# Kernel tuning notes

Measured on AMD Instinct MI355X. Metric: run time of the kernel, lower is better.

Reference implementation:

```python
import jax, jax.numpy as jnp
import numpy as np

B, T = 192, 50
VOCAB = 24000
EMBED = 300
HID2 = 2000          # 2*HIDDEN_SIZE
MAXOUT = 300         # DIMEN_MAXOUT_UNIT
QV = 300             # DIMEN_QUALITY_VECTOR
H2 = 100             # LSTM hidden


def setup_inputs():
    key = jax.random.key(0)
    ks = jax.random.split(key, 24)
    s = 0.02
    inp = {
        'dec_out': jax.random.normal(ks[0], (B, T, HID2), jnp.float32),
        'y': jax.random.randint(ks[1], (B, T), 0, VOCAB, jnp.int64 if jax.config.jax_enable_x64 else jnp.int32),
        'contex': jax.random.normal(ks[2], (B, T, HID2), jnp.float32),
        'embed_table': jax.random.normal(ks[3], (VOCAB, EMBED), jnp.float32) * s,
        'W1': jax.random.uniform(ks[4], (VOCAB, QV), jnp.float32),  # torch.rand
        'S_w': jax.random.normal(ks[5], (2 * MAXOUT, HID2), jnp.float32) * s,
        'S_b': jnp.zeros((2 * MAXOUT,), jnp.float32),
        'V_w': jax.random.normal(ks[6], (2 * MAXOUT, 2 * EMBED), jnp.float32) * s,
        'V_b': jnp.zeros((2 * MAXOUT,), jnp.float32),
        'C0_w': jax.random.normal(ks[7], (2 * MAXOUT, HID2), jnp.float32) * s,
        'C0_b': jnp.zeros((2 * MAXOUT,), jnp.float32),
        'W2_w': jax.random.normal(ks[8], (QV, MAXOUT), jnp.float32) * s,
        'W2_b': jnp.zeros((QV,), jnp.float32),
        'wih0': jax.random.normal(ks[9], (4 * H2, QV), jnp.float32) * s,
        'whh0': jax.random.normal(ks[10], (4 * H2, H2), jnp.float32) * s,
        'bih0': jnp.zeros((4 * H2,), jnp.float32),
        'bhh0': jnp.zeros((4 * H2,), jnp.float32),
        'wih1': jax.random.normal(ks[11], (4 * H2, H2), jnp.float32) * s,
        'whh1': jax.random.normal(ks[12], (4 * H2, H2), jnp.float32) * s,
        'bih1': jnp.zeros((4 * H2,), jnp.float32),
        'bhh1': jnp.zeros((4 * H2,), jnp.float32),
        'Wqe_w': jax.random.normal(ks[13], (1, H2), jnp.float32) * s,
        'Wqe_b': jnp.zeros((1,), jnp.float32),
    }
    return inp


def _lstm_layer(x, Wih, Whh, bih, bhh):
    # x: [B, T, D] -> outputs [B, T, H]; torch gate order i, f, g, o
    Bb = x.shape[0]
    H = Whh.shape[1]
    xT = jnp.swapaxes(x, 0, 1)  # [T, B, D]

    def step(carry, xt):
        h, c = carry
        g = xt @ Wih.T + h @ Whh.T + bih + bhh
        i, f, gg, o = jnp.split(g, 4, axis=-1)
        i = jax.nn.sigmoid(i); f = jax.nn.sigmoid(f)
        gg = jnp.tanh(gg); o = jax.nn.sigmoid(o)
        c = f * c + i * gg
        h = o * jnp.tanh(c)
        return (h, c), h

    h0 = jnp.zeros((Bb, H), x.dtype)
    (_, _), hs = jax.lax.scan(step, (h0, h0), xT)
    return jnp.swapaxes(hs, 0, 1)


def reference(dec_out, y, contex, embed_table, W1, S_w, S_b, V_w, V_b,
              C0_w, C0_b, W2_w, W2_b, wih0, whh0, bih0, bhh0,
              wih1, whh1, bih1, bhh1, Wqe_w, Wqe_b):
    Bb, Tt, _ = dec_out.shape
    embed = embed_table[y]  # [B, T, EMBED]
    idx = jnp.arange(Tt)
    li = jnp.where(idx == 0, 1, idx - 1)          # left neighbor (i==0 -> 1)
    ri = jnp.where(idx == Tt - 1, Tt - 2, idx + 1)  # right neighbor (i==T-1 -> T-2)
    tensor2 = jnp.concatenate([embed[:, li], embed[:, ri]], axis=-1)  # [B,T,600]
    t_long = (dec_out @ S_w.T + S_b) + (tensor2 @ V_w.T + V_b) + (contex @ C0_w.T + C0_b)
    # maxout over consecutive pairs: t[...,i] = max(t_long[...,2i], t_long[...,2i+1])
    t = t_long.reshape(Bb, Tt, MAXOUT, 2).max(axis=-1)
    a = t @ W2_w.T + W2_b                        # [B,T,QV]
    logits = a @ W1.T                            # [B,T,VOCAB]
    b = jax.nn.log_softmax(logits.reshape(Bb * Tt, -1), axis=1)
    quality = W1[y] * a                          # [B,T,QV]
    mask = (y == 0)
    index1 = jnp.where(mask.any(axis=1), mask.argmax(axis=1), Tt - 1)
    h = _lstm_layer(quality, wih0, whh0, bih0, bhh0)
    h = _lstm_layer(h, wih1, whh1, bih1, bhh1)   # [B,T,H2]
    s_sel = h[jnp.arange(Bb), index1]            # [B,H2]
    QE_score = jax.nn.sigmoid(s_sel @ Wqe_w.T + Wqe_b)  # [B,1]
    return (b, QE_score)
```

## Files before the change

### kernel.cpp

```cpp
#include <hip/hip_runtime.h>

typedef unsigned short u16;
typedef __attribute__((ext_vector_type(4))) float f32x4;
typedef __attribute__((ext_vector_type(8))) short bf16x8;
typedef __attribute__((ext_vector_type(4))) unsigned short u16x4;
typedef __attribute__((ext_vector_type(8))) unsigned short u16x8;

#define BT 9600
#define VOCAB 24000
#define NCB 188

__device__ __forceinline__ u16 f2b(float f){
  union { float f; unsigned u; } c; c.f = f;
  unsigned u = c.u;
  return (u16)((u + 0x7FFFu + ((u >> 16) & 1u)) >> 16);
}
__device__ __forceinline__ float b2f(u16 v){
  union { unsigned u; float f; } c; c.u = ((unsigned)v) << 16;
  return c.f;
}

#define GLD16(g, l) __builtin_amdgcn_global_load_lds( \
    (__attribute__((address_space(1))) void*)(g), \
    (__attribute__((address_space(3))) void*)(l), 16, 0, 0)

__device__ __forceinline__ void gemm_core(
    const u16* __restrict__ A, const u16* __restrict__ B,
    int K, int brow, int bcol, u16* As, u16* Bs, f32x4 acc[4][4])
{
  const int tid  = threadIdx.x & 255;
  const int w    = tid >> 6;
  const int lane = tid & 63;
  const int wm = w >> 1, wn = w & 1;

  const f32x4 fz = {0.f, 0.f, 0.f, 0.f};
  #pragma unroll
  for (int m = 0; m < 4; ++m)
    #pragma unroll
    for (int n = 0; n < 4; ++n) acc[m][n] = fz;

  const int nkt = K >> 6;

  auto stage = [&](int kt, int buf) {
    #pragma unroll
    for (int i = 0; i < 4; ++i) {
      int gl  = i * 256 + tid;
      int row = gl >> 3;
      int g   = (gl & 7) ^ (row & 7);
      const u16* ga = A + (size_t)(brow + row) * K + (kt << 6) + (g << 3);
      GLD16(ga, As + buf * 8192 + (size_t)(i * 256 + w * 64) * 8);
      const u16* gb = B + (size_t)(bcol + row) * K + (kt << 6) + (g << 3);
      GLD16(gb, Bs + buf * 8192 + (size_t)(i * 256 + w * 64) * 8);
    }
  };

  stage(0, 0);
  int cur = 0;
  for (int kt = 0; kt < nkt; ++kt) {
    if (kt + 1 < nkt) {
      stage(kt + 1, cur ^ 1);
      asm volatile("s_waitcnt vmcnt(8)" ::: "memory");
    } else {
      asm volatile("s_waitcnt vmcnt(0)" ::: "memory");
    }
    __builtin_amdgcn_s_barrier();
    asm volatile("" ::: "memory");
    const u16* Ab = As + cur * 8192;
    const u16* Bb = Bs + cur * 8192;
    #pragma unroll
    for (int kk = 0; kk < 2; ++kk) {
      bf16x8 af[4], bf[4];
      #pragma unroll
      for (int m = 0; m < 4; ++m) {
        int row = wm * 64 + m * 16 + (lane & 15);
        int g   = (kk * 4 + (lane >> 4)) ^ (row & 7);
        af[m] = *(const bf16x8*)(Ab + row * 64 + g * 8);
      }
      #pragma unroll
      for (int n = 0; n < 4; ++n) {
        int row = wn * 64 + n * 16 + (lane & 15);
        int g   = (kk * 4 + (lane >> 4)) ^ (row & 7);
        bf[n] = *(const bf16x8*)(Bb + row * 64 + g * 8);
      }
      #pragma unroll
      for (int m = 0; m < 4; ++m)
        #pragma unroll
        for (int n = 0; n < 4; ++n)
          acc[m][n] = __builtin_amdgcn_mfma_f32_16x16x32_bf16(af[m], bf[n], acc[m][n], 0, 0, 0);
    }
    asm volatile("" ::: "memory");
    __builtin_amdgcn_s_barrier();
    cur ^= 1;
  }
}

__device__ __forceinline__ void proj_epilogue(
    f32x4 acc[4][4], int brow, int bcol,
    const float* __restrict__ b1, const float* __restrict__ b2,
    float* __restrict__ out)
{
  int tid = threadIdx.x & 255;
  int lane = tid & 63, w = tid >> 6;
  int wm = w >> 1, wn = w & 1;
  #pragma unroll
  for (int m = 0; m < 4; ++m)
    #pragma unroll
    for (int n = 0; n < 4; ++n)
      #pragma unroll
      for (int r = 0; r < 4; ++r) {
        int row = brow + wm * 64 + m * 16 + ((lane >> 4) << 2) + r;
        int col = bcol + wn * 64 + n * 16 + (lane & 15);
        if (col < 400)
          out[(size_t)row * 400 + col] = acc[m][n][r] + b1[col] + b2[col];
      }
}

__device__ __forceinline__ void prep_main_body(
    const float* __restrict__ dec, const float* __restrict__ ctx,
    u16* __restrict__ Xcat, int tid)
{
  if (tid >= 9600 * 500) return;
  int r = tid / 500, k8 = (tid % 500) * 8;
  const float* src = (k8 < 2000) ? dec + (size_t)r * 2000 + k8
                                 : ctx + (size_t)r * 2000 + (k8 - 2000);
  const float4* s4 = (const float4*)src;
  float4 v0 = s4[0], v1 = s4[1];
  u16x8 o;
  o[0] = f2b(v0.x); o[1] = f2b(v0.y); o[2] = f2b(v0.z); o[3] = f2b(v0.w);
  o[4] = f2b(v1.x); o[5] = f2b(v1.y); o[6] = f2b(v1.z); o[7] = f2b(v1.w);
  *(u16x8*)(Xcat + (size_t)r * 4608 + k8) = o;
}

__device__ __forceinline__ void prep_emb_body(
    const int* __restrict__ y, const float* __restrict__ etab,
    u16* __restrict__ Xcat, int tid)
{
  if (tid >= 9600 * 152) return;
  int r = tid / 152, u = tid % 152;
  u16* xr = Xcat + (size_t)r * 4608;
  if (u >= 150) {
    int base = (u == 150) ? 4300 : 4604;
    u16x4 z; z[0] = 0; z[1] = 0; z[2] = 0; z[3] = 0;
    *(u16x4*)(xr + base) = z;
    return;
  }
  int t = r % 50;
  int side = u / 75, j4 = (u % 75) * 4;
  int tt = (side == 0) ? (t == 0 ? 1 : t - 1) : (t == 49 ? 48 : t + 1);
  int tok = y[r - t + tt];
  float4 v = *(const float4*)(etab + (size_t)tok * 300 + j4);
  u16x4 o; o[0] = f2b(v.x); o[1] = f2b(v.y); o[2] = f2b(v.z); o[3] = f2b(v.w);
  *(u16x4*)(xr + (side == 0 ? 4000 : 4304) + j4) = o;
}

__device__ __forceinline__ void wcat_body(
    const float* __restrict__ Sw, const float* __restrict__ C0w, const float* __restrict__ Vw,
    const float* __restrict__ Sb, const float* __restrict__ Vb, const float* __restrict__ C0b,
    u16* __restrict__ Wcat, float* __restrict__ biasc, int tid)
{
  if (tid >= 640 * 4608) return;
  int n = tid / 4608, k = tid % 4608;
  float v = 0.f;
  if (n < 600) {
    if (k < 2000)                  v = Sw[n * 2000 + k];
    else if (k < 4000)             v = C0w[n * 2000 + (k - 2000)];
    else if (k < 4300)             v = Vw[n * 600 + (k - 4000)];
    else if (k >= 4304 && k < 4604) v = Vw[n * 600 + 300 + (k - 4304)];
  }
  Wcat[tid] = f2b(v);
  if (k == 0) biasc[n] = (n < 600) ? (Sb[n] + Vb[n] + C0b[n]) : 0.f;
}

__device__ __forceinline__ void conv_body(
    const float* __restrict__ src, u16* __restrict__ dst,
    int srows, int scols, int drows, int dcols4, int tid)
{
  if (tid >= drows * dcols4) return;
  int r = tid / dcols4, c4 = (tid % dcols4) * 4;
  u16x4 o; o[0] = 0; o[1] = 0; o[2] = 0; o[3] = 0;
  if (r < srows && c4 < scols) {
    float4 v = *(const float4*)(src + (size_t)r * scols + c4);
    o[0] = f2b(v.x); o[1] = f2b(v.y); o[2] = f2b(v.z); o[3] = f2b(v.w);
  }
  *(u16x4*)(dst + (size_t)r * (dcols4 * 4) + c4) = o;
}

__global__ __launch_bounds__(256) void k_prep_all(
    const float* __restrict__ dec, const float* __restrict__ ctx,
    const int* __restrict__ y, const float* __restrict__ etab,
    const float* __restrict__ Sw, const float* __restrict__ C0w,
    const float* __restrict__ Vw, const float* __restrict__ Sb,
    const float* __restrict__ Vb, const float* __restrict__ C0b,
    const float* __restrict__ W1, const float* __restrict__ W2w,
    const float* __restrict__ wih0, const float* __restrict__ wih1,
    u16* __restrict__ Xcat, u16* __restrict__ Wcat, float* __restrict__ biasc,
    u16* __restrict__ W1b, u16* __restrict__ W2b,
    u16* __restrict__ wih0b, u16* __restrict__ wih1b)
{
  int bid = blockIdx.x, th = threadIdx.x;
  if (bid < 18750)      prep_main_body(dec, ctx, Xcat, bid * 256 + th);
  else if (bid < 24450) prep_emb_body(y, etab, Xcat, (bid - 18750) * 256 + th);
  else if (bid < 35970) wcat_body(Sw, C0w, Vw, Sb, Vb, C0b, Wcat, biasc, (bid - 24450) * 256 + th);
  else if (bid < 43490) conv_body(W1,   W1b,   24000, 300, 24064, 80, (bid - 35970) * 256 + th);
  else if (bid < 43610) conv_body(W2w,  W2b,   300,   300, 384,   80, (bid - 43490) * 256 + th);
  else if (bid < 43770) conv_body(wih0, wih0b, 400,   300, 512,   80, (bid - 43610) * 256 + th);
  else                  conv_body(wih1, wih1b, 400,   100, 512,   32, (bid - 43770) * 256 + th);
}

__global__ __launch_bounds__(256) void k_gemm_tlong(
    const u16* __restrict__ Xcat, const u16* __restrict__ Wcat,
    const float* __restrict__ biasc, u16* __restrict__ tb)
{
  __shared__ u16 As[16384], Bs[16384];
  f32x4 acc[4][4];
  int L = blockIdx.x;
  int xcd = L & 7, s = L >> 3;
  int yy = (s / 5) * 8 + xcd;
  int xx = s % 5;
  if (yy >= 75) return;
  int brow = yy * 128, bcol = xx * 128;
  gemm_core(Xcat, Wcat, 4608, brow, bcol, As, Bs, acc);
  int lane = threadIdx.x & 63, w = threadIdx.x >> 6;
  int wm = w >> 1, wn = w & 1;
  #pragma unroll
  for (int m = 0; m < 4; ++m)
    #pragma unroll
    for (int n = 0; n < 4; ++n)
      #pragma unroll
      for (int r = 0; r < 4; ++r) {
        int row = brow + wm * 64 + m * 16 + ((lane >> 4) << 2) + r;
        int col = bcol + wn * 64 + n * 16 + (lane & 15);
        float v = acc[m][n][r] + biasc[col];
        float o = __shfl_xor(v, 1);
        float t = fmaxf(v, o);
        if ((lane & 1) == 0)
          tb[(size_t)row * 320 + (col >> 1)] = f2b(t);
      }
}

__global__ __launch_bounds__(256) void k_gemm_a(
    const u16* __restrict__ tb, const u16* __restrict__ W2b,
    const float* __restrict__ W2bias, const float* __restrict__ W1,
    const int* __restrict__ y, u16* __restrict__ ab, u16* __restrict__ qb)
{
  __shared__ u16 As[16384], Bs[16384];
  f32x4 acc[4][4];
  int brow = blockIdx.y * 128, bcol = blockIdx.x * 128;
  gemm_core(tb, W2b, 320, brow, bcol, As, Bs, acc);
  int lane = threadIdx.x & 63, w = threadIdx.x >> 6;
  int wm = w >> 1, wn = w & 1;
  #pragma unroll
  for (int m = 0; m < 4; ++m)
    #pragma unroll
    for (int n = 0; n < 4; ++n)
      #pragma unroll
      for (int r = 0; r < 4; ++r) {
        int row = brow + wm * 64 + m * 16 + ((lane >> 4) << 2) + r;
        int col = bcol + wn * 64 + n * 16 + (lane & 15);
        if (col < 320) {
          float bias = (col < 300) ? W2bias[col] : 0.f;
          float a = acc[m][n][r] + bias;
          ab[(size_t)row * 320 + col] = f2b(a);
          float q = 0.f;
          if (col < 300) {
            int yv = y[row];
            q = a * W1[(size_t)yv * 300 + col];
          }
          qb[(size_t)row * 320 + col] = f2b(q);
        }
      }
}

__global__ __launch_bounds__(256) void k_s1(
    const u16* __restrict__ ab, const u16* __restrict__ W1b,
    u16* __restrict__ lb, float* __restrict__ part,
    const u16* __restrict__ qb, const u16* __restrict__ wih0b,
    const float* __restrict__ bih0, const float* __restrict__ bhh0,
    float* __restrict__ xp0)
{
  __shared__ u16 smem[32768];
  __shared__ float rowsum[128][2];
  f32x4 acc[4][4];
  int bid = blockIdx.x;
  if (bid < 300) {
    int brow = (bid / 4) * 128, bcol = (bid % 4) * 128;
    gemm_core(qb, wih0b, 320, brow, bcol, smem, smem + 16384, acc);
    proj_epilogue(acc, brow, bcol, bih0, bhh0, xp0);
    return;
  }
  int g = bid - 300;
  int brow = (g / NCB) * 128, bcol = (g % NCB) * 128;
  gemm_core(ab, W1b, 320, brow, bcol, smem, smem + 16384, acc);
  int lane = threadIdx.x & 63, w = threadIdx.x >> 6;
  int wm = w >> 1, wn = w & 1;
  #pragma unroll
  for (int m = 0; m < 4; ++m)
    #pragma unroll
    for (int r = 0; r < 4; ++r) {
      int lrow = wm * 64 + m * 16 + ((lane >> 4) << 2) + r;
      float es = 0.f;
      #pragma unroll
      for (int n = 0; n < 4; ++n) {
        int lcol = wn * 64 + n * 16 + (lane & 15);
        float v = acc[m][n][r];
        smem[lrow * 136 + lcol] = f2b(v);
        if (bcol + lcol < VOCAB) es += __expf(v);
      }
      es += __shfl_xor(es, 1); es += __shfl_xor(es, 2);
      es += __shfl_xor(es, 4); es += __shfl_xor(es, 8);
      if ((lane & 15) == 0) rowsum[lrow][wn] = es;
    }
  __syncthreads();
  if (threadIdx.x < 128)
    part[(size_t)(brow + threadIdx.x) * NCB + (g % NCB)] =
        rowsum[threadIdx.x][0] + rowsum[threadIdx.x][1];
  #pragma unroll
  for (int j = 0; j < 8; ++j) {
    int ch   = j * 256 + threadIdx.x;
    int rowl = ch >> 4;
    int c16  = (ch & 15) << 3;
    u16x8 v = *(const u16x8*)(smem + rowl * 136 + c16);
    *(u16x8*)(lb + (size_t)(brow + rowl) * 24064 + bcol + c16) = v;
  }
}

__device__ __forceinline__ void lstm0_body(
    const float* __restrict__ xp0, const float* __restrict__ whh0,
    u16* __restrict__ h0b, int b)
{
  int g = threadIdx.x;
  __shared__ float h[100];
  __shared__ float act[400];
  float wrow[100];
  if (g < 400) {
    const float4* wr = (const float4*)(whh0 + (size_t)g * 100);
    #pragma unroll
    for (int q = 0; q < 25; ++q) {
      float4 t = wr[q];
      wrow[4 * q] = t.x; wrow[4 * q + 1] = t.y; wrow[4 * q + 2] = t.z; wrow[4 * q + 3] = t.w;
    }
  }
  if (g < 100) h[g] = 0.f;
  float c = 0.f;
  __syncthreads();
  for (int t = 0; t < 50; ++t) {
    if (g < 400) {
      float s = xp0[(size_t)(b * 50 + t) * 400 + g];
      const float4* hv = (const float4*)h;
      #pragma unroll
      for (int q = 0; q < 25; ++q) {
        float4 hh = hv[q];
        s += wrow[4 * q] * hh.x + wrow[4 * q + 1] * hh.y
           + wrow[4 * q + 2] * hh.z + wrow[4 * q + 3] * hh.w;
      }
      act[g] = (g >= 200 && g < 300) ? tanhf(s) : 1.f / (1.f + __expf(-s));
    }
    __syncthreads();
    if (g < 100) {
      c = act[100 + g] * c + act[g] * act[200 + g];
      float hn = act[300 + g] * tanhf(c);
      h[g] = hn;
      h0b[(size_t)(b * 50 + t) * 128 + g] = f2b(hn);
    } else if (g < 128) {
      h0b[(size_t)(b * 50 + t) * 128 + g] = 0;
    }
    __syncthreads();
  }
}

__device__ __forceinline__ void lstm1_body(
    const float* __restrict__ xp1, const float* __restrict__ whh1,
    const int* __restrict__ y, const float* __restrict__ wqe,
    const float* __restrict__ wqeb, float* __restrict__ qout, int b)
{
  int g = threadIdx.x;
  __shared__ float h[100];
  __shared__ float act[400];
  __shared__ float hsel[100];
  __shared__ int idx1;
  float wrow[100];
  if (g < 400) {
    const float4* wr = (const float4*)(whh1 + (size_t)g * 100);
    #pragma unroll
    for (int q = 0; q < 25; ++q) {
      float4 t = wr[q];
      wrow[4 * q] = t.x; wrow[4 * q + 1] = t.y; wrow[4 * q + 2] = t.z; wrow[4 * q + 3] = t.w;
    }
  }
  if (g == 0) {
    int ix = 49;
    for (int t = 0; t < 50; ++t) { if (y[b * 50 + t] == 0) { ix = t; break; } }
    idx1 = ix;
  }
  if (g < 100) { h[g] = 0.f; hsel[g] = 0.f; }
  float c = 0.f;
  __syncthreads();
  for (int t = 0; t < 50; ++t) {
    if (g < 400) {
      float s = xp1[(size_t)(b * 50 + t) * 400 + g];
      const float4* hv = (const float4*)h;
      #pragma unroll
      for (int q = 0; q < 25; ++q) {
        float4 hh = hv[q];
        s += wrow[4 * q] * hh.x + wrow[4 * q + 1] * hh.y
           + wrow[4 * q + 2] * hh.z + wrow[4 * q + 3] * hh.w;
      }
      act[g] = (g >= 200 && g < 300) ? tanhf(s) : 1.f / (1.f + __expf(-s));
    }
    __syncthreads();
    if (g < 100) {
      c = act[100 + g] * c + act[g] * act[200 + g];
      float hn = act[300 + g] * tanhf(c);
      h[g] = hn;
      if (t == idx1) hsel[g] = hn;
    }
    __syncthreads();
  }
  if (g == 0) {
    float s = wqeb[0];
    for (int j = 0; j < 100; ++j) s += hsel[j] * wqe[j];
    qout[b] = 1.f / (1.f + __expf(-s));
  }
}

__device__ __forceinline__ void fixup_body(
    const u16* __restrict__ lb, const float* __restrict__ logl,
    float* __restrict__ out, int r0, int nrows, int bid, int nb, int nthreads)
{
  size_t i = (size_t)bid * nthreads + threadIdx.x;
  size_t stride = (size_t)nb * nthreads;
  const size_t total = (size_t)nrows * (VOCAB / 8);
  for (; i < total; i += stride) {
    size_t rowl = i / (VOCAB / 8);
    int c8 = (int)(i % (VOCAB / 8)) * 8;
    size_t row = r0 + rowl;
    float l = logl[row];
    u16x8 v = *(const u16x8*)(lb + row * 24064 + c8);
    float4 o0, o1;
    o0.x = b2f(v[0]) - l; o0.y = b2f(v[1]) - l; o0.z = b2f(v[2]) - l; o0.w = b2f(v[3]) - l;
    o1.x = b2f(v[4]) - l; o1.y = b2f(v[5]) - l; o1.z = b2f(v[6]) - l; o1.w = b2f(v[7]) - l;
    float* op = out + row * VOCAB + c8;
    *(float4*)op = o0;
    *(float4*)(op + 4) = o1;
  }
}

__global__ __launch_bounds__(512) void k_s2(
    const float* __restrict__ part, float* __restrict__ logl,
    const float* __restrict__ xp0, const float* __restrict__ whh0,
    u16* __restrict__ h0b)
{
  int bid = blockIdx.x;
  if (bid < 1200) {
    int row = bid * 8 + (threadIdx.x >> 6);
    int l = threadIdx.x & 63;
    const float* p = part + (size_t)row * NCB;
    float s = p[l] + p[l + 64] + (l < 60 ? p[l + 128] : 0.f);
    s += __shfl_xor(s, 1);  s += __shfl_xor(s, 2);  s += __shfl_xor(s, 4);
    s += __shfl_xor(s, 8);  s += __shfl_xor(s, 16); s += __shfl_xor(s, 32);
    if (l == 0) logl[row] = logf(s);
    return;
  }
  lstm0_body(xp0, whh0, h0b, bid - 1200);
}

__global__ __launch_bounds__(256) void k_s3(
    const u16* __restrict__ lb, const float* __restrict__ logl,
    float* __restrict__ out,
    const u16* __restrict__ h0b, const u16* __restrict__ wih1b,
    const float* __restrict__ bih1, const float* __restrict__ bhh1,
    float* __restrict__ xp1)
{
  int bid = blockIdx.x;
  if (bid < 3072) {
    fixup_body(lb, logl, out, 0, 6400, bid, 3072, 256);
    return;
  }
  __shared__ u16 As[16384], Bs[16384];
  f32x4 acc[4][4];
  int pb = bid - 3072;
  int brow = (pb / 4) * 128, bcol = (pb % 4) * 128;
  gemm_core(h0b, wih1b, 128, brow, bcol, As, Bs, acc);
  proj_epilogue(acc, brow, bcol, bih1, bhh1, xp1);
}

__global__ __launch_bounds__(512) void k_s4(
    const u16* __restrict__ lb, const float* __restrict__ logl,
    float* __restrict__ out,
    const float* __restrict__ xp1, const float* __restrict__ whh1,
    const int* __restrict__ y, const float* __restrict__ wqe,
    const float* __restrict__ wqeb, float* __restrict__ qout)
{
  int bid = blockIdx.x;
  if (bid < 192) {
    lstm1_body(xp1, whh1, y, wqe, wqeb, qout, bid);
    return;
  }
  fixup_body(lb, logl, out, 6400, 3200, bid - 192, 1024, 512);
}

__global__ __launch_bounds__(256) void k_gemm_logits_f32(
    const u16* __restrict__ ab, const u16* __restrict__ W1b,
    float* __restrict__ dout, float* __restrict__ part)
{
  __shared__ u16 As[16384], Bs[16384];
  __shared__ float rowsum[128][2];
  f32x4 acc[4][4];
  int brow = blockIdx.y * 128, bcol = blockIdx.x * 128;
  gemm_core(ab, W1b, 320, brow, bcol, As, Bs, acc);
  int lane = threadIdx.x & 63, w = threadIdx.x >> 6;
  int wm = w >> 1, wn = w & 1;
  #pragma unroll
  for (int m = 0; m < 4; ++m)
    #pragma unroll
    for (int r = 0; r < 4; ++r) {
      int lrow = wm * 64 + m * 16 + ((lane >> 4) << 2) + r;
      size_t grow = (size_t)(brow + lrow);
      float es = 0.f;
      #pragma unroll
      for (int n = 0; n < 4; ++n) {
        int col = bcol + wn * 64 + n * 16 + (lane & 15);
        float v = acc[m][n][r];
        if (col < VOCAB) { dout[grow * VOCAB + col] = v; es += __expf(v); }
      }
      es += __shfl_xor(es, 1); es += __shfl_xor(es, 2);
      es += __shfl_xor(es, 4); es += __shfl_xor(es, 8);
      if ((lane & 15) == 0) rowsum[lrow][wn] = es;
    }
  __syncthreads();
  if (threadIdx.x < 128)
    part[(size_t)(brow + threadIdx.x) * NCB + blockIdx.x] =
        rowsum[threadIdx.x][0] + rowsum[threadIdx.x][1];
}

__global__ __launch_bounds__(256) void k_gemm_proj(
    const u16* __restrict__ Ab, const u16* __restrict__ Bb, int K,
    const float* __restrict__ b1, const float* __restrict__ b2, float* __restrict__ out)
{
  __shared__ u16 As[16384], Bs[16384];
  f32x4 acc[4][4];
  int brow = blockIdx.y * 128, bcol = blockIdx.x * 128;
  gemm_core(Ab, Bb, K, brow, bcol, As, Bs, acc);
  proj_epilogue(acc, brow, bcol, b1, b2, out);
}

__global__ __launch_bounds__(256) void k_rowlog256(
    const float* __restrict__ part, float* __restrict__ logl)
{
  int row = blockIdx.x * 4 + (threadIdx.x >> 6);
  int l = threadIdx.x & 63;
  const float* p = part + (size_t)row * NCB;
  float s = p[l] + p[l + 64] + (l < 60 ? p[l + 128] : 0.f);
  s += __shfl_xor(s, 1);  s += __shfl_xor(s, 2);  s += __shfl_xor(s, 4);
  s += __shfl_xor(s, 8);  s += __shfl_xor(s, 16); s += __shfl_xor(s, 32);
  if (l == 0) logl[row] = logf(s);
}

__global__ __launch_bounds__(256) void k_fixup_f32(
    float4* __restrict__ out4, const float* __restrict__ logl)
{
  size_t i = (size_t)blockIdx.x * blockDim.x + threadIdx.x;
  size_t stride = (size_t)gridDim.x * blockDim.x;
  const size_t total = (size_t)BT * (VOCAB / 4);
  for (; i < total; i += stride) {
    size_t row = i / (VOCAB / 4);
    float l = logl[row];
    float4 v = out4[i];
    v.x -= l; v.y -= l; v.z -= l; v.w -= l;
    out4[i] = v;
  }
}

__global__ __launch_bounds__(512) void k_lstm0(
    const float* __restrict__ xp0, const float* __restrict__ whh0, u16* __restrict__ h0b)
{ lstm0_body(xp0, whh0, h0b, blockIdx.x); }

__global__ __launch_bounds__(512) void k_lstm1(
    const float* __restrict__ xp1, const float* __restrict__ whh1,
    const int* __restrict__ y, const float* __restrict__ wqe,
    const float* __restrict__ wqeb, float* __restrict__ qout)
{ lstm1_body(xp1, whh1, y, wqe, wqeb, qout, blockIdx.x); }

extern "C" void kernel_launch(void* const* d_in, const int* in_sizes, int n_in,
                              void* d_out, int out_size, void* d_ws, size_t ws_size,
                              hipStream_t stream) {
  const float* dec  = (const float*)d_in[0];
  const int*   y    = (const int*)d_in[1];
  const float* ctx  = (const float*)d_in[2];
  const float* etab = (const float*)d_in[3];
  const float* W1   = (const float*)d_in[4];
  const float* Sw   = (const float*)d_in[5];
  const float* Sb   = (const float*)d_in[6];
  const float* Vw   = (const float*)d_in[7];
  const float* Vb   = (const float*)d_in[8];
  const float* C0w  = (const float*)d_in[9];
  const float* C0b  = (const float*)d_in[10];
  const float* W2w  = (const float*)d_in[11];
  const float* W2bias = (const float*)d_in[12];
  const float* wih0 = (const float*)d_in[13];
  const float* whh0 = (const float*)d_in[14];
  const float* bih0 = (const float*)d_in[15];
  const float* bhh0 = (const float*)d_in[16];
  const float* wih1 = (const float*)d_in[17];
  const float* whh1 = (const float*)d_in[18];
  const float* bih1 = (const float*)d_in[19];
  const float* bhh1 = (const float*)d_in[20];
  const float* wqe  = (const float*)d_in[21];
  const float* wqeb = (const float*)d_in[22];

  char* ws = (char*)d_ws;
  u16*   Xcat  = (u16*)(ws + 0);
  u16*   Wcat  = (u16*)(ws + 88473600);
  float* biasc = (float*)(ws + 94371840);
  u16*   tb    = (u16*)(ws + 94374400);
  u16*   W2b   = (u16*)(ws + 100518400);
  u16*   ab    = (u16*)(ws + 100764160);
  u16*   qb    = (u16*)(ws + 106908160);
  u16*   W1b   = (u16*)(ws + 113052160);
  float* part  = (float*)(ws + 128453120);
  float* logl  = (float*)(ws + 135672320);
  u16*   wih0b = (u16*)(ws + 135710720);
  float* xp0   = (float*)(ws + 136038400);
  u16*   h0b   = (u16*)(ws + 151398400);
  u16*   wih1b = (u16*)(ws + 153856000);
  float* xp1   = (float*)(ws + 153987072);
  u16*   lb    = (u16*)(ws + 169347072);
  const size_t WS_NEED_BF16 = 169347072ull + 462028800ull;
  const bool use_bf16_logits = (ws_size >= WS_NEED_BF16);

  float* bout  = (float*)d_out;
  float* qeout = bout + (size_t)BT * VOCAB;

  k_prep_all<<<43834, 256, 0, stream>>>(dec, ctx, y, etab, Sw, C0w, Vw, Sb, Vb, C0b,
                                        W1, W2w, wih0, wih1,
                                        Xcat, Wcat, biasc, W1b, W2b, wih0b, wih1b);

  k_gemm_tlong<<<400, 256, 0, stream>>>(Xcat, Wcat, biasc, tb);
  k_gemm_a<<<dim3(3, 75), 256, 0, stream>>>(tb, W2b, W2bias, W1, y, ab, qb);

  if (use_bf16_logits) {
    k_s1<<<14400, 256, 0, stream>>>(ab, W1b, lb, part, qb, wih0b, bih0, bhh0, xp0);
    k_s2<<<1392, 512, 0, stream>>>(part, logl, xp0, whh0, h0b);
    k_s3<<<3372, 256, 0, stream>>>(lb, logl, bout, h0b, wih1b, bih1, bhh1, xp1);
    k_s4<<<1216, 512, 0, stream>>>(lb, logl, bout, xp1, whh1, y, wqe, wqeb, qeout);
  } else {
    k_gemm_logits_f32<<<dim3(NCB, 75), 256, 0, stream>>>(ab, W1b, bout, part);
    k_rowlog256<<<2400, 256, 0, stream>>>(part, logl);
    k_fixup_f32<<<4096, 256, 0, stream>>>((float4*)bout, logl);
    k_gemm_proj<<<dim3(4, 75), 256, 0, stream>>>(qb, wih0b, 320, bih0, bhh0, xp0);
    k_lstm0<<<192, 512, 0, stream>>>(xp0, whh0, h0b);
    k_gemm_proj<<<dim3(4, 75), 256, 0, stream>>>(h0b, wih1b, 128, bih1, bhh1, xp1);
    k_lstm1<<<192, 512, 0, stream>>>(xp1, whh1, y, wqe, wqeb, qeout);
  }
}
```

Measured before the change: 943.6 us.

## Use 256x256 tiles with 512 threads for logits and input-projection GEMMs

Replaces the 128x128, 256-thread GEMM in the fused logits/wih0 projection stage with a 256x256 tile computed by 512 threads (8 waves, each 128x64). This gives more data reuse per LDS load and cuts the number of per-row exp-sum partials in half. To support it, the ab/qb buffers are padded and zeroed to a 256-row multiple and the workspace layout is shifted. The larger tile doubles LDS use and raises register pressure, which may lower occupancy. The 9600-row edge is handled with guards.

After: 973.9 us. 3.2% more time.

```diff
diff --git a/kernel.cpp b/kernel.cpp
--- a/kernel.cpp
+++ b/kernel.cpp
@@ -9,6 +9,7 @@
 #define BT 9600
 #define VOCAB 24000
 #define NCB 188
+#define NCB2 94
 
 __device__ __forceinline__ u16 f2b(float f){
   union { float f; unsigned u; } c; c.f = f;
@@ -48,9 +49,9 @@
       int row = gl >> 3;
       int g   = (gl & 7) ^ (row & 7);
       const u16* ga = A + (size_t)(brow + row) * K + (kt << 6) + (g << 3);
-      GLD16(ga, As + buf * 8192 + (size_t)(i * 256 + w * 64) * 8);
+      GLD16(ga, As + buf * 8192 + gl * 8);
       const u16* gb = B + (size_t)(bcol + row) * K + (kt << 6) + (g << 3);
-      GLD16(gb, Bs + buf * 8192 + (size_t)(i * 256 + w * 64) * 8);
+      GLD16(gb, Bs + buf * 8192 + gl * 8);
     }
   };
 
@@ -87,6 +88,74 @@
         #pragma unroll
         for (int n = 0; n < 4; ++n)
           acc[m][n] = __builtin_amdgcn_mfma_f32_16x16x32_bf16(af[m], bf[n], acc[m][n], 0, 0, 0);
+    }
+    asm volatile("" ::: "memory");
+    __builtin_amdgcn_s_barrier();
+    cur ^= 1;
+  }
+}
+
+__device__ __forceinline__ void gemm_core256(
+    const u16* __restrict__ A, const u16* __restrict__ B,
+    int K, int brow, int bcol, u16* As, u16* Bs, f32x4 acc[8][4])
+{
+  const int tid  = threadIdx.x & 511;
+  const int w    = tid >> 6;
+  const int lane = tid & 63;
+  const int wr = w >> 2, wc = w & 3;
+
+  const f32x4 fz = {0.f, 0.f, 0.f, 0.f};
+  #pragma unroll
+  for (int m = 0; m < 8; ++m)
+    #pragma unroll
+    for (int n = 0; n < 4; ++n) acc[m][n] = fz;
+
+  const int nkt = K >> 6;
+
+  auto stage = [&](int kt, int buf) {
+    #pragma unroll
+    for (int i = 0; i < 4; ++i) {
+      int gl  = i * 512 + tid;
+      int row = gl >> 3;
+      int g   = (gl & 7) ^ (row & 7);
+      const u16* ga = A + (size_t)(brow + row) * K + (kt << 6) + (g << 3);
+      GLD16(ga, As + buf * 16384 + gl * 8);
+      const u16* gb = B + (size_t)(bcol + row) * K + (kt << 6) + (g << 3);
+      GLD16(gb, Bs + buf * 16384 + gl * 8);
+    }
+  };
+
+  stage(0, 0);
+  int cur = 0;
+  for (int kt = 0; kt < nkt; ++kt) {
+    if (kt + 1 < nkt) {
+      stage(kt + 1, cur ^ 1);
+      asm volatile("s_waitcnt vmcnt(8)" ::: "memory");
+    } else {
+      asm volatile("s_waitcnt vmcnt(0)" ::: "memory");
+    }
+    __builtin_amdgcn_s_barrier();
+    asm volatile("" ::: "memory");
+    const u16* Ab = As + cur * 16384;
+    const u16* Bb = Bs + cur * 16384;
+    #pragma unroll
+    for (int kk = 0; kk < 2; ++kk) {
+      bf16x8 bf[4];
+      #pragma unroll
+      for (int n = 0; n < 4; ++n) {
+        int row = wc * 64 + n * 16 + (lane & 15);
+        int g   = (kk * 4 + (lane >> 4)) ^ (row & 7);
+        bf[n] = *(const bf16x8*)(Bb + row * 64 + g * 8);
+      }
+      #pragma unroll
+      for (int m = 0; m < 8; ++m) {
+        int row = wr * 128 + m * 16 + (lane & 15);
+        int g   = (kk * 4 + (lane >> 4)) ^ (row & 7);
+        bf16x8 af = *(const bf16x8*)(Ab + row * 64 + g * 8);
+        #pragma unroll
+        for (int n = 0; n < 4; ++n)
+          acc[m][n] = __builtin_amdgcn_mfma_f32_16x16x32_bf16(af, bf[n], acc[m][n], 0, 0, 0);
+      }
     }
     asm volatile("" ::: "memory");
     __builtin_amdgcn_s_barrier();
@@ -185,6 +254,13 @@
   *(u16x4*)(dst + (size_t)r * (dcols4 * 4) + c4) = o;
 }
 
+__device__ __forceinline__ void zero_body(u16* __restrict__ dst, int n4, int tid)
+{
+  if (tid >= n4) return;
+  u16x4 z; z[0] = 0; z[1] = 0; z[2] = 0; z[3] = 0;
+  *(u16x4*)(dst + tid * 4) = z;
+}
+
 __global__ __launch_bounds__(256) void k_prep_all(
     const float* __restrict__ dec, const float* __restrict__ ctx,
     const int* __restrict__ y, const float* __restrict__ etab,
@@ -195,7 +271,8 @@
     const float* __restrict__ wih0, const float* __restrict__ wih1,
     u16* __restrict__ Xcat, u16* __restrict__ Wcat, float* __restrict__ biasc,
     u16* __restrict__ W1b, u16* __restrict__ W2b,
-    u16* __restrict__ wih0b, u16* __restrict__ wih1b)
+    u16* __restrict__ wih0b, u16* __restrict__ wih1b,
+    u16* __restrict__ ab, u16* __restrict__ qb)
 {
   int bid = blockIdx.x, th = threadIdx.x;
   if (bid < 18750)      prep_main_body(dec, ctx, Xcat, bid * 256 + th);
@@ -204,7 +281,9 @@
   else if (bid < 43490) conv_body(W1,   W1b,   24000, 300, 24064, 80, (bid - 35970) * 256 + th);
   else if (bid < 43610) conv_body(W2w,  W2b,   300,   300, 384,   80, (bid - 43490) * 256 + th);
   else if (bid < 43770) conv_body(wih0, wih0b, 400,   300, 512,   80, (bid - 43610) * 256 + th);
-  else                  conv_body(wih1, wih1b, 400,   100, 512,   32, (bid - 43770) * 256 + th);
+  else if (bid < 43834) conv_body(wih1, wih1b, 400,   100, 512,   32, (bid - 43770) * 256 + th);
+  else if (bid < 43874) zero_body(ab + 9600 * 320, 10240, (bid - 43834) * 256 + th);
+  else                  zero_body(qb + 9600 * 320, 10240, (bid - 43874) * 256 + th);
 }
 
 __global__ __launch_bounds__(256) void k_gemm_tlong(
@@ -271,56 +350,97 @@
       }
 }
 
-__global__ __launch_bounds__(256) void k_s1(
+__global__ __launch_bounds__(512, 2) void k_s1_256(
     const u16* __restrict__ ab, const u16* __restrict__ W1b,
     u16* __restrict__ lb, float* __restrict__ part,
     const u16* __restrict__ qb, const u16* __restrict__ wih0b,
     const float* __restrict__ bih0, const float* __restrict__ bhh0,
     float* __restrict__ xp0)
 {
-  __shared__ u16 smem[32768];
-  __shared__ float rowsum[128][2];
-  f32x4 acc[4][4];
+  __shared__ u16 smem[65536];
+  u16* As = smem;
+  u16* Bs = smem + 32768;
+  f32x4 acc[8][4];
+  const int tid = threadIdx.x;
+  const int lane = tid & 63, w = tid >> 6;
+  const int wr = w >> 2, wc = w & 3;
   int bid = blockIdx.x;
-  if (bid < 300) {
-    int brow = (bid / 4) * 128, bcol = (bid % 4) * 128;
-    gemm_core(qb, wih0b, 320, brow, bcol, smem, smem + 16384, acc);
-    proj_epilogue(acc, brow, bcol, bih0, bhh0, xp0);
+
+  if (bid < 76) {
+    int brow = (bid >> 1) * 256, bcol = (bid & 1) * 256;
+    gemm_core256(qb, wih0b, 320, brow, bcol, As, Bs, acc);
+    #pragma unroll
+    for (int m = 0; m < 8; ++m)
+      #pragma unroll
+      for (int n = 0; n < 4; ++n)
+        #pragma unroll
+        for (int r = 0; r < 4; ++r) {
+          int row = brow + wr * 128 + m * 16 + ((lane >> 4) << 2) + r;
+          int col = bcol + wc * 64 + n * 16 + (lane & 15);
+          if (row < 9600 && col < 400)
+            xp0[(size_t)row * 400 + col] = acc[m][n][r] + bih0[col] + bhh0[col];
+        }
     return;
   }
-  int g = bid - 300;
-  int brow = (g / NCB) * 128, bcol = (g % NCB) * 128;
-  gemm_core(ab, W1b, 320, brow, bcol, smem, smem + 16384, acc);
-  int lane = threadIdx.x & 63, w = threadIdx.x >> 6;
-  int wm = w >> 1, wn = w & 1;
+
+  int g = bid - 76;
+  int rb = g / NCB2, cb = g % NCB2;
+  int brow = rb * 256, bcol = cb * 256;
+  gemm_core256(ab, W1b, 320, brow, bcol, As, Bs, acc);
+
+  float* rs = (float*)smem;
   #pragma unroll
-  for (int m = 0; m < 4; ++m)
+  for (int m = 0; m < 8; ++m)
     #pragma unroll
     for (int r = 0; r < 4; ++r) {
-      int lrow = wm * 64 + m * 16 + ((lane >> 4) << 2) + r;
+      int lrow = wr * 128 + m * 16 + ((lane >> 4) << 2) + r;
       float es = 0.f;
       #pragma unroll
       for (int n = 0; n < 4; ++n) {
-        int lcol = wn * 64 + n * 16 + (lane & 15);
-        float v = acc[m][n][r];
-        smem[lrow * 136 + lcol] = f2b(v);
-        if (bcol + lcol < VOCAB) es += __expf(v);
+        int col = bcol + wc * 64 + n * 16 + (lane & 15);
+        if (col < VOCAB) es += __expf(acc[m][n][r]);
       }
       es += __shfl_xor(es, 1); es += __shfl_xor(es, 2);
       es += __shfl_xor(es, 4); es += __shfl_xor(es, 8);
-      if ((lane & 15) == 0) rowsum[lrow][wn] = es;
+      if ((lane & 15) == 0) rs[lrow * 4 + wc] = es;
     }
   __syncthreads();
-  if (threadIdx.x < 128)
-    part[(size_t)(brow + threadIdx.x) * NCB + (g % NCB)] =
-        rowsum[threadIdx.x][0] + rowsum[threadIdx.x][1];
+  if (tid < 256) {
+    int grow = brow + tid;
+    if (grow < 9600)
+      part[(size_t)grow * NCB2 + cb] =
+          rs[tid * 4] + rs[tid * 4 + 1] + rs[tid * 4 + 2] + rs[tid * 4 + 3];
+  }
+  __syncthreads();
+
+  u16* rp = smem + 2048;
   #pragma unroll
-  for (int j = 0; j < 8; ++j) {
-    int ch   = j * 256 + threadIdx.x;
-    int rowl = ch >> 4;
-    int c16  = (ch & 15) << 3;
-    u16x8 v = *(const u16x8*)(smem + rowl * 136 + c16);
-    *(u16x8*)(lb + (size_t)(brow + rowl) * 24064 + bcol + c16) = v;
+  for (int s = 0; s < 2; ++s) {
+    if (wr == s) {
+      #pragma unroll
+      for (int m = 0; m < 8; ++m)
+        #pragma unroll
+        for (int n = 0; n < 4; ++n)
+          #pragma unroll
+          for (int r = 0; r < 4; ++r) {
+            int lrow = m * 16 + ((lane >> 4) << 2) + r;
+            int col  = wc * 64 + n * 16 + (lane & 15);
+            rp[lrow * 264 + col] = f2b(acc[m][n][r]);
+          }
+    }
+    __syncthreads();
+    int rowbase = brow + s * 128;
+    #pragma unroll
+    for (int j = 0; j < 8; ++j) {
+      int ch = j * 512 + tid;
+      int rowl = ch >> 5, c8 = (ch & 31) << 3;
+      int grow = rowbase + rowl;
+      if (grow < 9600) {
+        u16x8 v = *(const u16x8*)(rp + rowl * 264 + c8);
+        *(u16x8*)(lb + (size_t)grow * 24064 + bcol + c8) = v;
+      }
+    }
+    __syncthreads();
   }
 }
 
@@ -454,8 +574,8 @@
   if (bid < 1200) {
     int row = bid * 8 + (threadIdx.x >> 6);
     int l = threadIdx.x & 63;
-    const float* p = part + (size_t)row * NCB;
-    float s = p[l] + p[l + 64] + (l < 60 ? p[l + 128] : 0.f);
+    const float* p = part + (size_t)row * NCB2;
+    float s = p[l] + (l < 30 ? p[l + 64] : 0.f);
     s += __shfl_xor(s, 1);  s += __shfl_xor(s, 2);  s += __shfl_xor(s, 4);
     s += __shfl_xor(s, 8);  s += __shfl_xor(s, 16); s += __shfl_xor(s, 32);
     if (l == 0) logl[row] = logf(s);
@@ -615,37 +735,39 @@
   u16*   tb    = (u16*)(ws + 94374400);
   u16*   W2b   = (u16*)(ws + 100518400);
   u16*   ab    = (u16*)(ws + 100764160);
-  u16*   qb    = (u16*)(ws + 106908160);
-  u16*   W1b   = (u16*)(ws + 113052160);
-  float* part  = (float*)(ws + 128453120);
-  float* logl  = (float*)(ws + 135672320);
-  u16*   wih0b = (u16*)(ws + 135710720);
-  float* xp0   = (float*)(ws + 136038400);
-  u16*   h0b   = (u16*)(ws + 151398400);
-  u16*   wih1b = (u16*)(ws + 153856000);
-  float* xp1   = (float*)(ws + 153987072);
-  u16*   lb    = (u16*)(ws + 169347072);
-  const size_t WS_NEED_BF16 = 169347072ull + 462028800ull;
+  u16*   qb    = (u16*)(ws + 106990080);
+  u16*   W1b   = (u16*)(ws + 113216000);
+  float* part  = (float*)(ws + 128616960);
+  float* logl  = (float*)(ws + 132226560);
+  u16*   wih0b = (u16*)(ws + 132264960);
+  float* xp0   = (float*)(ws + 132592640);
+  u16*   h0b   = (u16*)(ws + 147952640);
+  u16*   wih1b = (u16*)(ws + 150410240);
+  float* xp1   = (float*)(ws + 150541312);
+  u16*   lb    = (u16*)(ws + 165901312);
+  const size_t WS_NEED_BF16 = 165901312ull + 462028800ull;
   const bool use_bf16_logits = (ws_size >= WS_NEED_BF16);
 
   float* bout  = (float*)d_out;
   float* qeout = bout + (size_t)BT * VOCAB;
 
-  k_prep_all<<<43834, 256, 0, stream>>>(dec, ctx, y, etab, Sw, C0w, Vw, Sb, Vb, C0b,
+  k_prep_all<<<43914, 256, 0, stream>>>(dec, ctx, y, etab, Sw, C0w, Vw, Sb, Vb, C0b,
                                         W1, W2w, wih0, wih1,
-                                        Xcat, Wcat, biasc, W1b, W2b, wih0b, wih1b);
+                                        Xcat, Wcat, biasc, W1b, W2b, wih0b, wih1b,
+                                        ab, qb);
 
   k_gemm_tlong<<<400, 256, 0, stream>>>(Xcat, Wcat, biasc, tb);
   k_gemm_a<<<dim3(3, 75), 256, 0, stream>>>(tb, W2b, W2bias, W1, y, ab, qb);
 
   if (use_bf16_logits) {
-    k_s1<<<14400, 256, 0, stream>>>(ab, W1b, lb, part, qb, wih0b, bih0, bhh0, xp0);
+    k_s1_256<<<3648, 512, 0, stream>>>(ab, W1b, lb, part, qb, wih0b, bih0, bhh0, xp0);
     k_s2<<<1392, 512, 0, stream>>>(part, logl, xp0, whh0, h0b);
     k_s3<<<3372, 256, 0, stream>>>(lb, logl, bout, h0b, wih1b, bih1, bhh1, xp1);
     k_s4<<<1216, 512, 0, stream>>>(lb, logl, bout, xp1, whh1, y, wqe, wqeb, qeout);
   } else {
-    k_gemm_logits_f32<<<dim3(NCB, 75), 256, 0, stream>>>(ab, W1b, bout, part);
-    k_rowlog256<<<2400, 256, 0, stream>>>(part, logl);
+    float* part_fb = (float*)(ws + 165901312);
+    k_gemm_logits_f32<<<dim3(NCB, 75), 256, 0, stream>>>(ab, W1b, bout, part_fb);
+    k_rowlog256<<<2400, 256, 0, stream>>>(part_fb, logl);
     k_fixup_f32<<<4096, 256, 0, stream>>>((float4*)bout, logl);
     k_gemm_proj<<<dim3(4, 75), 256, 0, stream>>>(qb, wih0b, 320, bih0, bhh0, xp0);
     k_lstm0<<<192, 512, 0, stream>>>(xp0, whh0, h0b);
```
